# Optimization experiments

Measured on AMD Instinct MI355X. Metric: run time of the kernel, lower is better.

Reference implementation:

```python
import jax, jax.numpy as jnp
import numpy as np

D_MODEL = 1024
N_HEADS = 16


def setup_inputs() -> dict:
    key = jax.random.key(0)
    k1, k2, k3 = jax.random.split(key, 3)
    x = jax.random.normal(k1, (4, 2048, D_MODEL), dtype=jnp.float32)
    # torch nn.Linear(D, 3D): weight (3D, D), bias (3D)
    W = jax.random.normal(k2, (3 * D_MODEL, D_MODEL), dtype=jnp.float32) * (D_MODEL ** -0.5)
    b = jax.random.normal(k3, (3 * D_MODEL,), dtype=jnp.float32) * 0.01
    return {"x": x, "W": W, "b": b}


def reference(x, W, b):
    N, C, D = x.shape
    H = N_HEADS
    hd = D // H
    z = jnp.einsum("ncd,ed->nce", x, W) + b  # [N, C, 3D]
    k = z[:, :, :D].reshape(N, C, H, hd).transpose(0, 2, 1, 3)
    q = z[:, :, D:2 * D].reshape(N, C, H, hd).transpose(0, 2, 1, 3)
    v = z[:, :, 2 * D:].reshape(N, C, H, hd).transpose(0, 2, 1, 3)
    # NOTE: original scales by full model dim D, not head dim
    scores = jnp.einsum("nhqd,nhkd->nhqk", q, k) * (D ** -0.5)
    causal = jnp.tril(jnp.ones((C, C), dtype=bool))
    scores = jnp.where(causal[None, None], scores, -jnp.inf)
    attn = jax.nn.softmax(scores, axis=-1)
    out = jnp.einsum("nhqk,nhkd->nhqd", attn, v)
    return out.transpose(0, 2, 1, 3).reshape(N, C, D)
```

## Files before the change

kernel.cpp:

```cpp
#include <hip/hip_runtime.h>
#include <hip/hip_bf16.h>

typedef __bf16 bf16;
typedef __bf16 bf16x4 __attribute__((ext_vector_type(4)));
typedef __bf16 bf16x8 __attribute__((ext_vector_type(8)));
typedef float f32x4 __attribute__((ext_vector_type(4)));
typedef unsigned int u32x4 __attribute__((ext_vector_type(4)));

#define SEQ   2048
#define NBAT  4
#define DM    1024
#define NH    16
#define HD    64
#define E3    3072
#define E2    2048

__global__ void cvt2_bf16_kernel(const float* __restrict__ a, bf16* __restrict__ oa, int na8,
                                 const float* __restrict__ b, bf16* __restrict__ ob, int nb8) {
  const int stride = gridDim.x * blockDim.x;
  const int ntot = na8 + nb8;
  for (int i = blockIdx.x * blockDim.x + threadIdx.x; i < ntot; i += stride) {
    const float* src;
    bf16* dst;
    int j;
    if (i < na8) { src = a; dst = oa; j = i; }
    else         { src = b; dst = ob; j = i - na8; }
    const float4* p = (const float4*)(src + (size_t)j * 8);
    float4 x = p[0];
    float4 y = p[1];
    bf16x8 o;
    o[0] = (bf16)x.x; o[1] = (bf16)x.y; o[2] = (bf16)x.z; o[3] = (bf16)x.w;
    o[4] = (bf16)y.x; o[5] = (bf16)y.y; o[6] = (bf16)y.z; o[7] = (bf16)y.w;
    *(bf16x8*)(dst + (size_t)j * 8) = o;
  }
}

#define BM 128
#define BN 128
#define BK 32
#define KSTEPS (DM / BK)

__global__ __launch_bounds__(256, 2) void qkv_gemm_kernel(
    const bf16* __restrict__ A, const bf16* __restrict__ B,
    const float* __restrict__ bias, bf16* __restrict__ Z2, bf16* __restrict__ VT)
{
  __shared__ bf16 sA[2][BM * BK];
  __shared__ bf16 sB[2][BN * BK];

  const int tid  = threadIdx.x;
  const int lane = tid & 63;
  const int w    = tid >> 6;
  const int wr   = w >> 1;
  const int wc   = w & 1;
  const int m0   = blockIdx.x * BM;
  const int n0   = blockIdx.y * BN;

  const f32x4 z4 = {0.f, 0.f, 0.f, 0.f};
  f32x4 acc[4][4];
#pragma unroll
  for (int i = 0; i < 4; ++i)
#pragma unroll
    for (int j = 0; j < 4; ++j)
      acc[i][j] = z4;

  const int srow = w * 32 + (lane >> 2);
  const int skk  = (lane & 3) * 8;
  const bf16* gA = A + (size_t)m0 * DM;
  const bf16* gB = B + (size_t)n0 * DM;

  auto stage = [&](int buf, int t) {
    const int k0 = t * BK;
#pragma unroll
    for (int c = 0; c < 2; ++c)
      __builtin_amdgcn_global_load_lds(
          (const __attribute__((address_space(1))) unsigned int*)(gA + (size_t)(srow + c * 16) * DM + k0 + skk),
          (__attribute__((address_space(3))) unsigned int*)(&sA[buf][w * 1024 + c * 512]),
          16, 0, 0);
#pragma unroll
    for (int c = 0; c < 2; ++c)
      __builtin_amdgcn_global_load_lds(
          (const __attribute__((address_space(1))) unsigned int*)(gB + (size_t)(srow + c * 16) * DM + k0 + skk),
          (__attribute__((address_space(3))) unsigned int*)(&sB[buf][w * 1024 + c * 512]),
          16, 0, 0);
  };

  stage(0, 0);
  int cur = 0;
  const int arow = wr * 64 + (lane & 15);
  const int brow = wc * 64 + (lane & 15);
  const int kf   = (lane >> 4) * 8;

  for (int t = 0; t < KSTEPS; ++t) {
    __syncthreads();
    if (t + 1 < KSTEPS) stage(cur ^ 1, t + 1);
    bf16x8 af[4], bfr[4];
#pragma unroll
    for (int i = 0; i < 4; ++i)
      af[i] = *(const bf16x8*)&sA[cur][(arow + i * 16) * BK + kf];
#pragma unroll
    for (int j = 0; j < 4; ++j)
      bfr[j] = *(const bf16x8*)&sB[cur][(brow + j * 16) * BK + kf];
#pragma unroll
    for (int i = 0; i < 4; ++i)
#pragma unroll
      for (int j = 0; j < 4; ++j)
        acc[i][j] = __builtin_amdgcn_mfma_f32_16x16x32_bf16(af[i], bfr[j], acc[i][j], 0, 0, 0);
    cur ^= 1;
  }

  if (n0 < 2048) {
#pragma unroll
    for (int i = 0; i < 4; ++i) {
#pragma unroll
      for (int j = 0; j < 4; ++j) {
        const int col = n0 + wc * 64 + j * 16 + (lane & 15);
        const float bb = bias[col];
#pragma unroll
        for (int r = 0; r < 4; ++r) {
          const int row = m0 + wr * 64 + i * 16 + (lane >> 4) * 4 + r;
          Z2[(size_t)row * E2 + col] = (bf16)(acc[i][j][r] + bb);
        }
      }
    }
  } else {
#pragma unroll
    for (int i = 0; i < 4; ++i) {
      const int rowb = m0 + wr * 64 + i * 16 + (lane >> 4) * 4;
      const int nb   = rowb >> 11;
      const int k    = rowb & 2047;
      const int ksig = (k & ~63) | (k & 32) | (((k >> 2) & 3) << 3) | (((k >> 4) & 1) << 2);
#pragma unroll
      for (int j = 0; j < 4; ++j) {
        const int col  = n0 + wc * 64 + j * 16 + (lane & 15);
        const float bb = bias[col];
        const int colv = col - 2048;
        const int h    = colv >> 6;
        const int d    = colv & 63;
        bf16x4 v4;
#pragma unroll
        for (int r = 0; r < 4; ++r) v4[r] = (bf16)(acc[i][j][r] + bb);
        *(bf16x4*)&VT[(((size_t)nb * NH + h) * HD + d) * SEQ + ksig] = v4;
      }
    }
  }
}

#define QB 128
#define KB 64
#define NQT (SEQ / QB)

__global__ __launch_bounds__(256, 2) void attn_kernel(
    const bf16* __restrict__ Z2, const bf16* __restrict__ VT, float* __restrict__ out)
{
  __shared__ bf16 sK[2][KB][64];
  __shared__ bf16 sVT[2][HD][64];

  const int tid   = threadIdx.x;
  const int lane  = tid & 63;
  const int w     = tid >> 6;
  const int l15   = lane & 15;
  const int lhi   = lane >> 4;
  const int l7    = l15 & 7;
  const int e2    = l15 >> 3;

  const int flat  = blockIdx.x;
  const int xcd   = flat & 7;
  const int idx   = flat >> 3;
  const int ctx   = xcd * 8 + (idx & 7);
  const int pairb = idx >> 3;
  const int h     = ctx & 15;
  const int n     = ctx >> 4;

  const size_t zb2 = (size_t)n * SEQ * E2;
  const size_t vtb = ((size_t)n * NH + h) * HD * SEQ;
  const int kcol0 = h * HD;
  const int qcol0 = DM + h * HD;

  const f32x4 z4 = {0.f, 0.f, 0.f, 0.f};
  const f32x4 neg4 = {-1e32f, -1e32f, -1e32f, -1e32f};
  const float scale = 0.03125f;
  const float L2E   = 1.4426950408889634f;
  const float SL2E  = scale * L2E;

  const u32x4 onesu = {0x3F803F80u, 0x3F803F80u, 0x3F803F80u, 0x3F803F80u};
  const bf16x8 onesf = __builtin_bit_cast(bf16x8, onesu);

  const int krow_in = lane >> 3;
  const int kdblk   = ((lane & 7) ^ (lane >> 3)) * 8;

  const size_t ob = (size_t)n * SEQ * DM;

  auto stageK = [&](int t, int buf) {
#pragma unroll
    for (int c = 0; c < 2; ++c) {
      const int cc = 2 * w + c;
      __builtin_amdgcn_global_load_lds(
          (const __attribute__((address_space(1))) unsigned int*)(
              Z2 + zb2 + (size_t)(t * KB + 8 * cc + krow_in) * E2 + kcol0 + kdblk),
          (__attribute__((address_space(3))) unsigned int*)(&sK[buf][8 * cc][0]),
          16, 0, 0);
    }
  };
  auto stageV = [&](int t, int buf) {
#pragma unroll
    for (int c = 0; c < 2; ++c) {
      const int cc   = 2 * w + c;
      const int dsrc = 8 * cc + (lane >> 3);
      const int blk  = (lane & 7) ^ ((dsrc ^ (dsrc >> 3)) & 7);
      __builtin_amdgcn_global_load_lds(
          (const __attribute__((address_space(1))) unsigned int*)(
              VT + vtb + (size_t)dsrc * SEQ + t * KB + blk * 8),
          (__attribute__((address_space(3))) unsigned int*)(&sVT[buf][8 * cc][0]),
          16, 0, 0);
    }
  };

#pragma unroll 1
  for (int phase = 0; phase < 2; ++phase) {
    const int qtile = phase == 0 ? pairb : (NQT - 1 - pairb);
    const int qwave = qtile * QB + w * 32;
    const int T     = 2 * qtile + 2;

    bf16x8 qf[2][2];
#pragma unroll
    for (int qs = 0; qs < 2; ++qs) {
      const int qrow = qwave + qs * 16 + l15;
#pragma unroll
      for (int kk = 0; kk < 2; ++kk)
        qf[qs][kk] = *(const bf16x8*)&Z2[zb2 + (size_t)qrow * E2 + qcol0 + kk * 32 + lhi * 8];
    }

    f32x4 accO[2][4];
    f32x4 accL[2];
#pragma unroll
    for (int qs = 0; qs < 2; ++qs) {
#pragma unroll
      for (int dt = 0; dt < 4; ++dt) accO[qs][dt] = z4;
      accL[qs] = z4;
    }

    stageK(0, 0);
    stageV(0, 0);
    __syncthreads();

#pragma unroll 1
    for (int t = 0; t < T; ++t) {
      const int cur = t & 1;
      if (t + 1 < T) { stageK(t + 1, cur ^ 1); stageV(t + 1, cur ^ 1); }

      f32x4 st[2][4];
      __builtin_amdgcn_s_setprio(1);
#pragma unroll
      for (int kt = 0; kt < 4; ++kt) {
        const int blk0 = (lhi ^ l7) * 8;
        const int blk1 = ((4 + lhi) ^ l7) * 8;
        bf16x8 kf0 = *(const bf16x8*)&sK[cur][kt * 16 + l15][blk0];
        bf16x8 kf1 = *(const bf16x8*)&sK[cur][kt * 16 + l15][blk1];
#pragma unroll
        for (int qs = 0; qs < 2; ++qs) {
          st[qs][kt] = __builtin_amdgcn_mfma_f32_16x16x32_bf16(kf0, qf[qs][0], z4, 0, 0, 0);
          st[qs][kt] = __builtin_amdgcn_mfma_f32_16x16x32_bf16(kf1, qf[qs][1], st[qs][kt], 0, 0, 0);
        }
      }
      __builtin_amdgcn_s_setprio(0);

      if (t >= 2 * qtile) {
        const int tb = 4 * (t - 2 * qtile);
#pragma unroll
        for (int qs = 0; qs < 2; ++qs) {
          const int dgq = 2 * w + qs;
#pragma unroll
          for (int kt = 0; kt < 4; ++kt) {
            const int fg = tb + kt;
            if (fg > dgq) st[qs][kt] = neg4;
            else if (fg == dgq) {
#pragma unroll
              for (int r = 0; r < 4; ++r)
                if (lhi * 4 + r > l15) st[qs][kt][r] = -1e32f;
            }
          }
        }
      }

      bf16x8 pb[2][2];
#pragma unroll
      for (int qs = 0; qs < 2; ++qs)
#pragma unroll
        for (int c = 0; c < 2; ++c) {
          u32x4 pu;
#pragma unroll
          for (int i = 0; i < 4; ++i) {
            const int kt = 2 * c + (i >> 1);
            const int r  = (2 * i) & 3;
            const float p0 = exp2f(st[qs][kt][r]     * SL2E);
            const float p1 = exp2f(st[qs][kt][r + 1] * SL2E);
            const bf16 b0v = (bf16)p0;
            const bf16 b1v = (bf16)p1;
            pu[i] = (unsigned int)__builtin_bit_cast(unsigned short, b0v)
                  | ((unsigned int)__builtin_bit_cast(unsigned short, b1v) << 16);
          }
          pb[qs][c] = __builtin_bit_cast(bf16x8, pu);
        }

      __builtin_amdgcn_s_setprio(1);
#pragma unroll
      for (int c = 0; c < 2; ++c)
#pragma unroll
        for (int qs = 0; qs < 2; ++qs)
          accL[qs] = __builtin_amdgcn_mfma_f32_16x16x32_bf16(onesf, pb[qs][c], accL[qs], 0, 0, 0);

#pragma unroll
      for (int c = 0; c < 2; ++c) {
#pragma unroll
        for (int dt = 0; dt < 4; ++dt) {
          const int idxv = ((4 * c + lhi) ^ (l7 ^ ((2 * dt + e2) & 7))) << 3;
          const bf16x8 av = *(const bf16x8*)&sVT[cur][dt * 16 + l15][idxv];
#pragma unroll
          for (int qs = 0; qs < 2; ++qs)
            accO[qs][dt] = __builtin_amdgcn_mfma_f32_16x16x32_bf16(av, pb[qs][c], accO[qs][dt], 0, 0, 0);
        }
      }
      __builtin_amdgcn_s_setprio(0);

      __syncthreads();
    }

#pragma unroll
    for (int qs = 0; qs < 2; ++qs) {
      const float inv  = 1.f / accL[qs][0];
      const int   qrow = qwave + qs * 16 + l15;
#pragma unroll
      for (int dt = 0; dt < 4; ++dt) {
        float4 o;
        o.x = accO[qs][dt][0] * inv;
        o.y = accO[qs][dt][1] * inv;
        o.z = accO[qs][dt][2] * inv;
        o.w = accO[qs][dt][3] * inv;
        *(float4*)&out[ob + (size_t)qrow * DM + h * HD + dt * 16 + lhi * 4] = o;
      }
    }
  }
}

extern "C" void kernel_launch(void* const* d_in, const int* in_sizes, int n_in,
                              void* d_out, int out_size, void* d_ws, size_t ws_size,
                              hipStream_t stream) {
  const float* x    = (const float*)d_in[0];
  const float* W    = (const float*)d_in[1];
  const float* bias = (const float*)d_in[2];
  float* out = (float*)d_out;

  bf16* xb = (bf16*)d_ws;
  bf16* Wb = xb + (size_t)NBAT * SEQ * DM;
  bf16* Z2 = Wb + (size_t)E3 * DM;
  bf16* VT = Z2 + (size_t)NBAT * SEQ * E2;

  cvt2_bf16_kernel<<<1536, 256, 0, stream>>>(x, xb, NBAT * SEQ * DM / 8,
                                             W, Wb, E3 * DM / 8);

  dim3 g1(NBAT * SEQ / BM, E3 / BN);
  qkv_gemm_kernel<<<g1, 256, 0, stream>>>(xb, Wb, bias, Z2, VT);

  attn_kernel<<<512, 256, 0, stream>>>(Z2, VT, out);
}
```

Measured before the change: 154.9 us.

## Halve attention query tile, double grid, fold softmax scale into Q projection

The attention kernel now processes 64-query tiles with one 16-row slice per wave instead of two, doubling the block count to 1024 and raising the occupancy hint to 4 blocks per CU. The causal mask simplifies to the final key tile only. The softmax scale times log2(e) is folded into the Q columns in the GEMM epilogue, which removes a multiply per score. The smaller tile improves parallelism and load balance but halves reuse of each staged K/V tile, so more K/V traffic goes through LDS.

```diff
diff --git a/kernel.cpp b/kernel.cpp
--- a/kernel.cpp
+++ b/kernel.cpp
@@ -14,6 +14,8 @@
 #define HD    64
 #define E3    3072
 #define E2    2048
+
+#define SL2E_C 0.04508422f
 
 __global__ void cvt2_bf16_kernel(const float* __restrict__ a, bf16* __restrict__ oa, int na8,
                                  const float* __restrict__ b, bf16* __restrict__ ob, int nb8) {
@@ -109,6 +111,7 @@
   }
 
   if (n0 < 2048) {
+    const float sc = (n0 >= 1024) ? SL2E_C : 1.0f;
 #pragma unroll
     for (int i = 0; i < 4; ++i) {
 #pragma unroll
@@ -118,7 +121,7 @@
 #pragma unroll
         for (int r = 0; r < 4; ++r) {
           const int row = m0 + wr * 64 + i * 16 + (lane >> 4) * 4 + r;
-          Z2[(size_t)row * E2 + col] = (bf16)(acc[i][j][r] + bb);
+          Z2[(size_t)row * E2 + col] = (bf16)((acc[i][j][r] + bb) * sc);
         }
       }
     }
@@ -145,11 +148,11 @@
   }
 }
 
-#define QB 128
+#define QB 64
 #define KB 64
 #define NQT (SEQ / QB)
 
-__global__ __launch_bounds__(256, 2) void attn_kernel(
+__global__ __launch_bounds__(256, 4) void attn_kernel(
     const bf16* __restrict__ Z2, const bf16* __restrict__ VT, float* __restrict__ out)
 {
   __shared__ bf16 sK[2][KB][64];
@@ -165,9 +168,9 @@
 
   const int flat  = blockIdx.x;
   const int xcd   = flat & 7;
-  const int idx   = flat >> 3;
-  const int ctx   = xcd * 8 + (idx & 7);
-  const int pairb = idx >> 3;
+  const int u     = flat >> 3;
+  const int ctx   = xcd * 8 + (u & 7);
+  const int pairb = u >> 3;
   const int h     = ctx & 15;
   const int n     = ctx >> 4;
 
@@ -178,9 +181,6 @@
 
   const f32x4 z4 = {0.f, 0.f, 0.f, 0.f};
   const f32x4 neg4 = {-1e32f, -1e32f, -1e32f, -1e32f};
-  const float scale = 0.03125f;
-  const float L2E   = 1.4426950408889634f;
-  const float SL2E  = scale * L2E;
 
   const u32x4 onesu = {0x3F803F80u, 0x3F803F80u, 0x3F803F80u, 0x3F803F80u};
   const bf16x8 onesf = __builtin_bit_cast(bf16x8, onesu);
@@ -218,26 +218,22 @@
 #pragma unroll 1
   for (int phase = 0; phase < 2; ++phase) {
     const int qtile = phase == 0 ? pairb : (NQT - 1 - pairb);
-    const int qwave = qtile * QB + w * 32;
-    const int T     = 2 * qtile + 2;
-
-    bf16x8 qf[2][2];
-#pragma unroll
-    for (int qs = 0; qs < 2; ++qs) {
-      const int qrow = qwave + qs * 16 + l15;
+    const int qwave = qtile * QB + w * 16;
+    const int T     = qtile + 1;
+
+    bf16x8 qf[2];
+    {
+      const int qrow = qwave + l15;
 #pragma unroll
       for (int kk = 0; kk < 2; ++kk)
-        qf[qs][kk] = *(const bf16x8*)&Z2[zb2 + (size_t)qrow * E2 + qcol0 + kk * 32 + lhi * 8];
-    }
-
-    f32x4 accO[2][4];
-    f32x4 accL[2];
-#pragma unroll
-    for (int qs = 0; qs < 2; ++qs) {
-#pragma unroll
-      for (int dt = 0; dt < 4; ++dt) accO[qs][dt] = z4;
-      accL[qs] = z4;
-    }
+        qf[kk] = *(const bf16x8*)&Z2[zb2 + (size_t)qrow * E2 + qcol0 + kk * 32 + lhi * 8];
+    }
+
+    f32x4 accO[4];
+    f32x4 accL;
+#pragma unroll
+    for (int dt = 0; dt < 4; ++dt) accO[dt] = z4;
+    accL = z4;
 
     stageK(0, 0);
     stageV(0, 0);
@@ -248,66 +244,53 @@
       const int cur = t & 1;
       if (t + 1 < T) { stageK(t + 1, cur ^ 1); stageV(t + 1, cur ^ 1); }
 
-      f32x4 st[2][4];
+      f32x4 st[4];
       __builtin_amdgcn_s_setprio(1);
 #pragma unroll
       for (int kt = 0; kt < 4; ++kt) {
         const int blk0 = (lhi ^ l7) * 8;
         const int blk1 = ((4 + lhi) ^ l7) * 8;
         bf16x8 kf0 = *(const bf16x8*)&sK[cur][kt * 16 + l15][blk0];
+        st[kt] = __builtin_amdgcn_mfma_f32_16x16x32_bf16(kf0, qf[0], z4, 0, 0, 0);
         bf16x8 kf1 = *(const bf16x8*)&sK[cur][kt * 16 + l15][blk1];
-#pragma unroll
-        for (int qs = 0; qs < 2; ++qs) {
-          st[qs][kt] = __builtin_amdgcn_mfma_f32_16x16x32_bf16(kf0, qf[qs][0], z4, 0, 0, 0);
-          st[qs][kt] = __builtin_amdgcn_mfma_f32_16x16x32_bf16(kf1, qf[qs][1], st[qs][kt], 0, 0, 0);
-        }
+        st[kt] = __builtin_amdgcn_mfma_f32_16x16x32_bf16(kf1, qf[1], st[kt], 0, 0, 0);
       }
       __builtin_amdgcn_s_setprio(0);
 
-      if (t >= 2 * qtile) {
-        const int tb = 4 * (t - 2 * qtile);
-#pragma unroll
-        for (int qs = 0; qs < 2; ++qs) {
-          const int dgq = 2 * w + qs;
-#pragma unroll
-          for (int kt = 0; kt < 4; ++kt) {
-            const int fg = tb + kt;
-            if (fg > dgq) st[qs][kt] = neg4;
-            else if (fg == dgq) {
-#pragma unroll
-              for (int r = 0; r < 4; ++r)
-                if (lhi * 4 + r > l15) st[qs][kt][r] = -1e32f;
-            }
+      if (t == T - 1) {
+#pragma unroll
+        for (int kt = 0; kt < 4; ++kt) {
+          if (kt > w) st[kt] = neg4;
+          else if (kt == w) {
+#pragma unroll
+            for (int r = 0; r < 4; ++r)
+              if (lhi * 4 + r > l15) st[kt][r] = -1e32f;
           }
         }
       }
 
-      bf16x8 pb[2][2];
-#pragma unroll
-      for (int qs = 0; qs < 2; ++qs)
-#pragma unroll
-        for (int c = 0; c < 2; ++c) {
-          u32x4 pu;
-#pragma unroll
-          for (int i = 0; i < 4; ++i) {
-            const int kt = 2 * c + (i >> 1);
-            const int r  = (2 * i) & 3;
-            const float p0 = exp2f(st[qs][kt][r]     * SL2E);
-            const float p1 = exp2f(st[qs][kt][r + 1] * SL2E);
-            const bf16 b0v = (bf16)p0;
-            const bf16 b1v = (bf16)p1;
-            pu[i] = (unsigned int)__builtin_bit_cast(unsigned short, b0v)
-                  | ((unsigned int)__builtin_bit_cast(unsigned short, b1v) << 16);
-          }
-          pb[qs][c] = __builtin_bit_cast(bf16x8, pu);
+      bf16x8 pb[2];
+#pragma unroll
+      for (int c = 0; c < 2; ++c) {
+        u32x4 pu;
+#pragma unroll
+        for (int i = 0; i < 4; ++i) {
+          const int kt = 2 * c + (i >> 1);
+          const int r  = (2 * i) & 3;
+          const float p0 = exp2f(st[kt][r]);
+          const float p1 = exp2f(st[kt][r + 1]);
+          const bf16 b0v = (bf16)p0;
+          const bf16 b1v = (bf16)p1;
+          pu[i] = (unsigned int)__builtin_bit_cast(unsigned short, b0v)
+                | ((unsigned int)__builtin_bit_cast(unsigned short, b1v) << 16);
         }
+        pb[c] = __builtin_bit_cast(bf16x8, pu);
+      }
 
       __builtin_amdgcn_s_setprio(1);
 #pragma unroll
       for (int c = 0; c < 2; ++c)
-#pragma unroll
-        for (int qs = 0; qs < 2; ++qs)
-          accL[qs] = __builtin_amdgcn_mfma_f32_16x16x32_bf16(onesf, pb[qs][c], accL[qs], 0, 0, 0);
+        accL = __builtin_amdgcn_mfma_f32_16x16x32_bf16(onesf, pb[c], accL, 0, 0, 0);
 
 #pragma unroll
       for (int c = 0; c < 2; ++c) {
@@ -315,9 +298,7 @@
         for (int dt = 0; dt < 4; ++dt) {
           const int idxv = ((4 * c + lhi) ^ (l7 ^ ((2 * dt + e2) & 7))) << 3;
           const bf16x8 av = *(const bf16x8*)&sVT[cur][dt * 16 + l15][idxv];
-#pragma unroll
-          for (int qs = 0; qs < 2; ++qs)
-            accO[qs][dt] = __builtin_amdgcn_mfma_f32_16x16x32_bf16(av, pb[qs][c], accO[qs][dt], 0, 0, 0);
+          accO[dt] = __builtin_amdgcn_mfma_f32_16x16x32_bf16(av, pb[c], accO[dt], 0, 0, 0);
         }
       }
       __builtin_amdgcn_s_setprio(0);
@@ -325,17 +306,16 @@
       __syncthreads();
     }
 
-#pragma unroll
-    for (int qs = 0; qs < 2; ++qs) {
-      const float inv  = 1.f / accL[qs][0];
-      const int   qrow = qwave + qs * 16 + l15;
+    {
+      const float inv  = 1.f / accL[0];
+      const int   qrow = qwave + l15;
 #pragma unroll
       for (int dt = 0; dt < 4; ++dt) {
         float4 o;
-        o.x = accO[qs][dt][0] * inv;
-        o.y = accO[qs][dt][1] * inv;
-        o.z = accO[qs][dt][2] * inv;
-        o.w = accO[qs][dt][3] * inv;
+        o.x = accO[dt][0] * inv;
+        o.y = accO[dt][1] * inv;
+        o.z = accO[dt][2] * inv;
+        o.w = accO[dt][3] * inv;
         *(float4*)&out[ob + (size_t)qrow * DM + h * HD + dt * 16 + lhi * 4] = o;
       }
     }
@@ -361,5 +341,5 @@
   dim3 g1(NBAT * SEQ / BM, E3 / BN);
   qkv_gemm_kernel<<<g1, 256, 0, stream>>>(xb, Wb, bias, Z2, VT);
 
-  attn_kernel<<<512, 256, 0, stream>>>(Z2, VT, out);
+  attn_kernel<<<1024, 256, 0, stream>>>(Z2, VT, out);
 }
```

New measurement: 148.1 us. -4.4%, faster.
